# Optimization experiments

Measured on AMD Instinct MI355X. Metric: run time of the kernel, lower is better.

Reference implementation:

```python
import jax, jax.numpy as jnp
import numpy as np

N_NODES, N_LAYERS, D = 4096, 8, 128


def setup_inputs() -> dict:
    key = jax.random.key(0)
    k1, k2, k3 = jax.random.split(key, 3)
    feature = jax.random.normal(k1, (N_NODES, N_LAYERS, D), dtype=jnp.float32)
    W = jax.random.uniform(k2, (D, D), dtype=jnp.float32)
    adj = jax.random.randint(k3, (N_LAYERS, N_NODES, N_NODES), 0, 2, dtype=jnp.int32)
    return {"feature": feature, "W": W, "adj": adj}


def reference(feature, W, adj):
    # feature: [N, L, D]; W: [D, D]; adj: [L, N, N] with 0/1 entries.
    # Original loop: for i, for l, for j in neighbors(i) U {i}:
    #     ret[j, l, :] = (W @ feature[i, l, :]) / sqrt(d_i * d_j)   # OVERWRITE
    # => final ret[j, l] uses the LAST source i with adj[l,i,j]==1 or i==j.
    L, N = adj.shape[0], adj.shape[1]
    i_idx = jnp.arange(N)
    # mask[l, i, j]: source i writes to destination j at layer l
    mask = (adj == 1) | (i_idx[:, None] == i_idx[None, :])
    # last (largest) source index per (l, j); diagonal guarantees >= 0
    src = jnp.max(jnp.where(mask, i_idx[:, None], -1), axis=1)          # [L, N]
    deg = jnp.sum(adj, axis=2).astype(feature.dtype) + 1.0              # [L, N]
    # shared tiny GEMM applied to all (node, layer) features
    Wf = jnp.einsum('de,nle->lnd', W, feature)                          # [L, N, D]
    gathered = jnp.take_along_axis(Wf, src[:, :, None], axis=1)         # [L, N, D]
    d_src = jnp.take_along_axis(deg, src, axis=1)                       # [L, N]
    scale = 1.0 / jnp.sqrt(d_src * deg)                                 # [L, N]
    ret = jnp.transpose(gathered * scale[:, :, None], (1, 0, 2))        # [N, L, D]
    return ret
```

## Files before the change

kernel.cpp:

```cpp
#include <hip/hip_runtime.h>
#include <cstddef>

#define NN 4096
#define NL 8
#define ND 128

#define SRC_BLOCKS (NL * (NN / 256))
#define ROWS 4
#define WF_BLOCKS 256

typedef int   int4v   __attribute__((ext_vector_type(4)));
typedef float float4v __attribute__((ext_vector_type(4)));


__global__ __launch_bounds__(256) void degsrc_kernel(const int* __restrict__ adj,
                                                     float* __restrict__ deg,
                                                     int* __restrict__ src) {
  if (blockIdx.x < SRC_BLOCKS) {
    const int bid = blockIdx.x;
    const int l = bid >> 4;
    const int j = ((bid & 15) << 8) + threadIdx.x;
    const int* __restrict__ A = adj + (size_t)l * NN * NN + j;
    int cur = j;
    bool found = false;
    int itop = NN - 1;
    while (true) {
      int ibot = itop - 31;
      if (ibot < 0) ibot = 0;
      int best = -1;
#pragma unroll
      for (int k = 0; k < 32; ++k) {
        int i = itop - k;
        int a = (i >= ibot) ? A[(size_t)i * NN] : 0;
        int c = (a != 0 && i > j) ? i : -1;
        if (c > best) best = c;
      }
      if (!found && best >= 0) { cur = best; found = true; }
      bool done = found || (ibot <= j + 1);
      if (__syncthreads_and((int)done)) break;
      itop = ibot - 1;
    }
    src[l * NN + j] = cur;
  } else {
    const size_t row = (size_t)(blockIdx.x - SRC_BLOCKS) * ROWS +
                       (threadIdx.x >> 6);
    const int lane = threadIdx.x & 63;
    const int4v* __restrict__ p =
        reinterpret_cast<const int4v*>(adj + row * (size_t)NN);
    int s = 0;
#pragma unroll
    for (int k = 0; k < 16; ++k) {
      int4v v = __builtin_nontemporal_load(&p[lane + k * 64]);
      s += v.x + v.y + v.z + v.w;
    }
    for (int off = 32; off > 0; off >>= 1) s += __shfl_down(s, off, 64);
    if (lane == 0) deg[row] = (float)s + 1.0f;
  }
}

__global__ __launch_bounds__(256) void compact_kernel(const int* __restrict__ src,
                                                      int* __restrict__ wl,
                                                      int* __restrict__ count) {
  const int l = blockIdx.x;
  __shared__ unsigned mask[NN / 32];
  __shared__ int cnt;
  if (threadIdx.x < NN / 32) mask[threadIdx.x] = 0u;
  if (threadIdx.x == 0) cnt = 0;
  __syncthreads();
  for (int k = threadIdx.x; k < NN; k += 256) {
    int s = src[l * NN + k];
    atomicOr(&mask[s >> 5], 1u << (s & 31));
  }
  __syncthreads();
  if (threadIdx.x < NN / 32) {
    unsigned m = mask[threadIdx.x];
    while (m) {
      int b = __ffs(m) - 1;
      m &= m - 1;
      int pos = atomicAdd(&cnt, 1);
      wl[l * NN + pos] = (threadIdx.x << 5) | b;
    }
  }
  __syncthreads();
  if (threadIdx.x == 0) count[l] = cnt;
}

__global__ __launch_bounds__(128) void wf_kernel(const float* __restrict__ feature,
                                                 const float* __restrict__ W,
                                                 const int* __restrict__ wl,
                                                 const int* __restrict__ count,
                                                 float* __restrict__ Wf) {
  __shared__ int base[NL + 1];
  __shared__ float fbuf[ND];
  if (threadIdx.x == 0) {
    int s = 0;
    for (int l = 0; l < NL; ++l) { base[l] = s; s += count[l]; }
    base[NL] = s;
  }
  __syncthreads();
  const int total = base[NL];
  const int d = threadIdx.x;

  for (int t = blockIdx.x; t < total; t += WF_BLOCKS) {
    int l = 0;
    while (t >= base[l + 1]) ++l;
    const int i = wl[l * NN + (t - base[l])];
    if (threadIdx.x < 32)
      reinterpret_cast<float4v*>(fbuf)[threadIdx.x] =
          reinterpret_cast<const float4v*>(
              feature + ((size_t)i * NL + l) * ND)[threadIdx.x];
    __syncthreads();
    float acc = 0.0f;
#pragma unroll 8
    for (int eq = 0; eq < 32; ++eq) {
      float4v wv = reinterpret_cast<const float4v*>(W + (size_t)d * ND)[eq];
      float4v fv = reinterpret_cast<const float4v*>(fbuf)[eq];
      acc += wv.x * fv.x + wv.y * fv.y + wv.z * fv.z + wv.w * fv.w;
    }
    Wf[((size_t)l * NN + i) * ND + d] = acc;
    __syncthreads();
  }
}

__global__ __launch_bounds__(256) void out_kernel(const float* __restrict__ Wf,
                                                  const float* __restrict__ deg,
                                                  const int* __restrict__ src,
                                                  float* __restrict__ out) {
  const int g = blockIdx.x * 256 + threadIdx.x;
  const int q = g & 31;
  const int jl = g >> 5;
  const int l = jl & 7;
  const int j = jl >> 3;
  const int s = src[l * NN + j];
  const float sc = rsqrtf(deg[l * NN + s] * deg[l * NN + j]);
  float4v v = reinterpret_cast<const float4v*>(Wf + ((size_t)l * NN + s) * ND)[q];
  v.x *= sc; v.y *= sc; v.z *= sc; v.w *= sc;
  __builtin_nontemporal_store(v, reinterpret_cast<float4v*>(out) + g);
}

extern "C" void kernel_launch(void* const* d_in, const int* in_sizes, int n_in,
                              void* d_out, int out_size, void* d_ws,
                              size_t ws_size, hipStream_t stream) {
  const float* feature = (const float*)d_in[0];
  const float* W       = (const float*)d_in[1];
  const int*   adj     = (const int*)d_in[2];
  float* out = (float*)d_out;

  char* ws = (char*)d_ws;
  float* deg   = (float*)(ws);
  int*   src   = (int*)(ws + 131072);
  int*   wl    = (int*)(ws + 262144);
  int*   count = (int*)(ws + 393216);
  float* Wf    = (float*)(ws + 409600);

  degsrc_kernel<<<SRC_BLOCKS + NL * NN / ROWS, 256, 0, stream>>>(adj, deg, src);
  compact_kernel<<<NL, 256, 0, stream>>>(src, wl, count);
  wf_kernel<<<WF_BLOCKS, 128, 0, stream>>>(feature, W, wl, count, Wf);
  out_kernel<<<NN * NL * ND / 4 / 256, 256, 0, stream>>>(Wf, deg, src, out);
}
```

Baseline: 101.4 us.

## Fuse compaction, Wf GEMM and output scatter into one per-chunk kernel

New measurement: 102.5 us. No clear change (+1.0%).

```diff
diff --git a/kernel.cpp b/kernel.cpp
--- a/kernel.cpp
+++ b/kernel.cpp
@@ -7,7 +7,9 @@
 
 #define SRC_BLOCKS (NL * (NN / 256))
 #define ROWS 4
-#define WF_BLOCKS 256
+
+#define CHUNK 128
+#define BATCH 16
 
 typedef int   int4v   __attribute__((ext_vector_type(4)));
 typedef float float4v __attribute__((ext_vector_type(4)));
@@ -58,84 +60,109 @@
   }
 }
 
-__global__ __launch_bounds__(256) void compact_kernel(const int* __restrict__ src,
-                                                      int* __restrict__ wl,
-                                                      int* __restrict__ count) {
-  const int l = blockIdx.x;
+__global__ __launch_bounds__(256) void outfused_kernel(
+    const float* __restrict__ feature, const float* __restrict__ W,
+    const float* __restrict__ deg, const int* __restrict__ src,
+    float* __restrict__ out) {
   __shared__ unsigned mask[NN / 32];
-  __shared__ int cnt;
-  if (threadIdx.x < NN / 32) mask[threadIdx.x] = 0u;
-  if (threadIdx.x == 0) cnt = 0;
+  __shared__ int ps[128];
+  __shared__ int list[CHUNK];
+  __shared__ int srcs[CHUNK];
+  __shared__ float scj[CHUNK];
+  __shared__ int smap[CHUNK];
+  __shared__ float fb[BATCH][ND];
+  __shared__ float wf[BATCH][ND];
+
+  const int t = threadIdx.x;
+  const int l = blockIdx.y;
+  const int jbase = blockIdx.x * CHUNK;
+
+  const int d = t & 127;
+  float4v wreg[32];
+#pragma unroll
+  for (int q = 0; q < 32; ++q)
+    wreg[q] = reinterpret_cast<const float4v*>(W)[(size_t)d * 32 + q];
+
+  if (t < 128) mask[t] = 0u;
   __syncthreads();
-  for (int k = threadIdx.x; k < NN; k += 256) {
-    int s = src[l * NN + k];
+  if (t < CHUNK) {
+    int j = jbase + t;
+    int s = src[l * NN + j];
+    srcs[t] = s;
     atomicOr(&mask[s >> 5], 1u << (s & 31));
+    scj[t] = rsqrtf(deg[l * NN + s] * deg[l * NN + j]);
   }
   __syncthreads();
-  if (threadIdx.x < NN / 32) {
-    unsigned m = mask[threadIdx.x];
+
+  int pc = 0;
+  if (t < 128) { pc = __popc(mask[t]); ps[t] = pc; }
+  __syncthreads();
+  for (int off = 1; off < 128; off <<= 1) {
+    int v = 0;
+    if (t < 128 && t >= off) v = ps[t - off];
+    __syncthreads();
+    if (t < 128 && t >= off) ps[t] += v;
+    __syncthreads();
+  }
+  if (t < 128) {
+    unsigned m = mask[t];
+    int pos = ps[t] - pc;
     while (m) {
       int b = __ffs(m) - 1;
       m &= m - 1;
-      int pos = atomicAdd(&cnt, 1);
-      wl[l * NN + pos] = (threadIdx.x << 5) | b;
+      list[pos++] = (t << 5) | b;
     }
   }
   __syncthreads();
-  if (threadIdx.x == 0) count[l] = cnt;
-}
+  const int cnt = ps[127];
 
-__global__ __launch_bounds__(128) void wf_kernel(const float* __restrict__ feature,
-                                                 const float* __restrict__ W,
-                                                 const int* __restrict__ wl,
-                                                 const int* __restrict__ count,
-                                                 float* __restrict__ Wf) {
-  __shared__ int base[NL + 1];
-  __shared__ float fbuf[ND];
-  if (threadIdx.x == 0) {
-    int s = 0;
-    for (int l = 0; l < NL; ++l) { base[l] = s; s += count[l]; }
-    base[NL] = s;
+  const int h = t >> 7;
+
+  for (int b0 = 0; b0 < cnt; b0 += BATCH) {
+    const int nb = min(BATCH, cnt - b0);
+    __syncthreads();
+
+    for (int idx = t; idx < nb * 32; idx += 256) {
+      int k = idx >> 5, q = idx & 31;
+      int i = list[b0 + k];
+      reinterpret_cast<float4v*>(fb[k])[q] =
+          reinterpret_cast<const float4v*>(feature + ((size_t)i * NL + l) * ND)[q];
+    }
+    if (t < CHUNK) {
+      int s = srcs[t], sl = -1;
+      for (int k = 0; k < nb; ++k)
+        if (list[b0 + k] == s) sl = k;
+      smap[t] = sl;
+    }
+    __syncthreads();
+
+    const int kend = min(h * 8 + 8, nb);
+    for (int k = h * 8; k < kend; ++k) {
+      float acc = 0.0f;
+#pragma unroll
+      for (int q = 0; q < 32; ++q) {
+        float4v f = reinterpret_cast<const float4v*>(fb[k])[q];
+        acc += wreg[q].x * f.x + wreg[q].y * f.y + wreg[q].z * f.z +
+               wreg[q].w * f.w;
+      }
+      wf[k][d] = acc;
+    }
+    __syncthreads();
+
+    for (int r0 = 0; r0 < CHUNK; r0 += 8) {
+      const int r = r0 + (t >> 5);
+      const int q = t & 31;
+      const int sl = smap[r];
+      if (sl >= 0) {
+        float4v v = reinterpret_cast<const float4v*>(wf[sl])[q];
+        const float sc = scj[r];
+        v.x *= sc; v.y *= sc; v.z *= sc; v.w *= sc;
+        __builtin_nontemporal_store(
+            v, reinterpret_cast<float4v*>(out) +
+                   ((size_t)(jbase + r) * NL + l) * 32 + q);
+      }
+    }
   }
-  __syncthreads();
-  const int total = base[NL];
-  const int d = threadIdx.x;
-
-  for (int t = blockIdx.x; t < total; t += WF_BLOCKS) {
-    int l = 0;
-    while (t >= base[l + 1]) ++l;
-    const int i = wl[l * NN + (t - base[l])];
-    if (threadIdx.x < 32)
-      reinterpret_cast<float4v*>(fbuf)[threadIdx.x] =
-          reinterpret_cast<const float4v*>(
-              feature + ((size_t)i * NL + l) * ND)[threadIdx.x];
-    __syncthreads();
-    float acc = 0.0f;
-#pragma unroll 8
-    for (int eq = 0; eq < 32; ++eq) {
-      float4v wv = reinterpret_cast<const float4v*>(W + (size_t)d * ND)[eq];
-      float4v fv = reinterpret_cast<const float4v*>(fbuf)[eq];
-      acc += wv.x * fv.x + wv.y * fv.y + wv.z * fv.z + wv.w * fv.w;
-    }
-    Wf[((size_t)l * NN + i) * ND + d] = acc;
-    __syncthreads();
-  }
-}
-
-__global__ __launch_bounds__(256) void out_kernel(const float* __restrict__ Wf,
-                                                  const float* __restrict__ deg,
-                                                  const int* __restrict__ src,
-                                                  float* __restrict__ out) {
-  const int g = blockIdx.x * 256 + threadIdx.x;
-  const int q = g & 31;
-  const int jl = g >> 5;
-  const int l = jl & 7;
-  const int j = jl >> 3;
-  const int s = src[l * NN + j];
-  const float sc = rsqrtf(deg[l * NN + s] * deg[l * NN + j]);
-  float4v v = reinterpret_cast<const float4v*>(Wf + ((size_t)l * NN + s) * ND)[q];
-  v.x *= sc; v.y *= sc; v.z *= sc; v.w *= sc;
-  __builtin_nontemporal_store(v, reinterpret_cast<float4v*>(out) + g);
 }
 
 extern "C" void kernel_launch(void* const* d_in, const int* in_sizes, int n_in,
@@ -147,14 +174,10 @@
   float* out = (float*)d_out;
 
   char* ws = (char*)d_ws;
-  float* deg   = (float*)(ws);
-  int*   src   = (int*)(ws + 131072);
-  int*   wl    = (int*)(ws + 262144);
-  int*   count = (int*)(ws + 393216);
-  float* Wf    = (float*)(ws + 409600);
+  float* deg = (float*)(ws);
+  int*   src = (int*)(ws + 131072);
 
   degsrc_kernel<<<SRC_BLOCKS + NL * NN / ROWS, 256, 0, stream>>>(adj, deg, src);
-  compact_kernel<<<NL, 256, 0, stream>>>(src, wl, count);
-  wf_kernel<<<WF_BLOCKS, 128, 0, stream>>>(feature, W, wl, count, Wf);
-  out_kernel<<<NN * NL * ND / 4 / 256, 256, 0, stream>>>(Wf, deg, src, out);
+  outfused_kernel<<<dim3(NN / CHUNK, NL), 256, 0, stream>>>(feature, W, deg,
+                                                            src, out);
 }
```
